# Optimization experiments

Hardware: AMD Instinct MI355X
Metric: run time of the kernel (lower is better)

## Reference

```python
import jax, jax.numpy as jnp
import numpy as np

N, E, IN_DIM, EMBED_DIM, HID_DIM = 10000, 320000, 128, 128, 64
NEG_SLOPE = 0.2


def setup_inputs() -> dict:
    key = jax.random.key(0)
    ks = jax.random.split(key, 7)
    x = jax.random.normal(ks[0], (N, IN_DIM), dtype=jnp.float32)
    edge_index = jax.random.randint(ks[1], (2, E), 0, N, dtype=jnp.int64)
    dense_w = jax.random.normal(ks[2], (IN_DIM, EMBED_DIM), dtype=jnp.float32) / np.sqrt(IN_DIM)
    dense_b = jnp.zeros((EMBED_DIM,), dtype=jnp.float32)
    gat_w = jax.random.normal(ks[3], (EMBED_DIM, HID_DIM), dtype=jnp.float32) / np.sqrt(EMBED_DIM)
    att_src = jax.random.normal(ks[4], (HID_DIM,), dtype=jnp.float32) * 0.1
    att_dst = jax.random.normal(ks[5], (HID_DIM,), dtype=jnp.float32) * 0.1
    gat_b = jnp.zeros((HID_DIM,), dtype=jnp.float32)
    return {"x": x, "edge_index": edge_index, "dense_w": dense_w, "dense_b": dense_b,
            "gat_w": gat_w, "att_src": att_src, "att_dst": att_dst, "gat_b": gat_b}


def reference(x, edge_index, dense_w, dense_b, gat_w, att_src, att_dst, gat_b):
    n = x.shape[0]
    # dense + relu
    h = jax.nn.relu(x @ dense_w + dense_b)            # [N, embed]
    # GATConv (heads=1): linear transform
    z = h @ gat_w                                     # [N, hid]
    # add self loops (PyG default)
    loops = jnp.arange(n, dtype=edge_index.dtype)
    src = jnp.concatenate([edge_index[0], loops])     # [E+N] message source j
    dst = jnp.concatenate([edge_index[1], loops])     # [E+N] message target i
    a_src = z @ att_src                               # [N]
    a_dst = z @ att_dst                               # [N]
    e = jax.nn.leaky_relu(a_src[src] + a_dst[dst], NEG_SLOPE)  # [E+N]
    # segment softmax over incoming edges of each target node
    m = jax.ops.segment_max(e, dst, num_segments=n)
    ex = jnp.exp(e - m[dst])
    denom = jax.ops.segment_sum(ex, dst, num_segments=n)
    alpha = ex / denom[dst]                           # [E+N]
    embed_x = jax.ops.segment_sum(alpha[:, None] * z[src], dst, num_segments=n) + gat_b  # [N, hid]
    # pairwise sigmoid similarity
    sim = jax.nn.sigmoid(embed_x @ embed_x.T)         # [N, N]
    return sim, embed_x
```

## Files before the change

### kernel.cpp

```cpp
#include <hip/hip_runtime.h>
#include <math.h>

#define N_NODES 10000
#define E_EDGES 320000
#define IN_DIM 128
#define EMB 128
#define HID 64
#define NEG_SLOPE 0.2f

typedef __attribute__((ext_vector_type(8))) short short8;
typedef __attribute__((ext_vector_type(4))) short short4_t;
typedef __attribute__((ext_vector_type(4))) float floatx4;

__device__ __forceinline__ short f2bf(float f) {
    unsigned u = __float_as_uint(f);
    unsigned r = u + 0x7fffu + ((u >> 16) & 1u);
    return (short)(r >> 16);
}

__global__ __launch_bounds__(256) void dense_gat_kernel(
    const float* __restrict__ x, const float* __restrict__ dw,
    const float* __restrict__ db, const float* __restrict__ gw,
    float* __restrict__ z)
{
    __shared__ float xs[16][IN_DIM];
    __shared__ float hs[16][EMB];
    const int t = threadIdx.x;
    const int row0 = blockIdx.x * 16;

    #pragma unroll
    for (int r = 0; r < 2; ++r) {
        const int idx = t + r * 256;
        const int row = idx >> 5, c4 = idx & 31;
        *(floatx4*)&xs[row][c4 * 4] =
            *(const floatx4*)&x[(row0 + row) * IN_DIM + c4 * 4];
    }
    __syncthreads();

    {
        const int col = t & 127, rb = (t >> 7) * 8;
        float acc[8];
        const float bias = db[col];
        #pragma unroll
        for (int r = 0; r < 8; ++r) acc[r] = bias;
        for (int j = 0; j < IN_DIM; ++j) {
            const float wj = dw[j * EMB + col];
            #pragma unroll
            for (int r = 0; r < 8; ++r) acc[r] = fmaf(xs[rb + r][j], wj, acc[r]);
        }
        #pragma unroll
        for (int r = 0; r < 8; ++r) hs[rb + r][col] = fmaxf(acc[r], 0.f);
    }
    __syncthreads();

    {
        const int col = t & 63, rb = (t >> 6) * 4;
        float acc[4] = {0.f, 0.f, 0.f, 0.f};
        for (int k = 0; k < EMB; ++k) {
            const float g = gw[k * HID + col];
            #pragma unroll
            for (int r = 0; r < 4; ++r) acc[r] = fmaf(hs[rb + r][k], g, acc[r]);
        }
        #pragma unroll
        for (int r = 0; r < 4; ++r) z[(row0 + rb + r) * HID + col] = acc[r];
    }
}

__global__ __launch_bounds__(256) void att_kernel(
    const float* __restrict__ z, const float* __restrict__ asv,
    const float* __restrict__ adv, float* __restrict__ a_src,
    float* __restrict__ a_dst)
{
    const int wid  = (blockIdx.x * blockDim.x + threadIdx.x) >> 6;
    const int lane = threadIdx.x & 63;
    if (wid >= N_NODES) return;
    const float zv = z[wid * HID + lane];
    float ps = zv * asv[lane];
    float pd = zv * adv[lane];
    #pragma unroll
    for (int off = 32; off > 0; off >>= 1) {
        ps += __shfl_down(ps, off, 64);
        pd += __shfl_down(pd, off, 64);
    }
    if (lane == 0) { a_src[wid] = ps; a_dst[wid] = pd; }
}

__global__ __launch_bounds__(256) void count_kernel(
    const int* __restrict__ ei, int* __restrict__ cnt)
{
    const int e = blockIdx.x * blockDim.x + threadIdx.x;
    const int total = E_EDGES + N_NODES;
    if (e >= total) return;
    int s, d;
    if (e < E_EDGES) { s = ei[e]; d = ei[E_EDGES + e]; }
    else             { s = d = e - E_EDGES; }
    if ((unsigned)s >= N_NODES || (unsigned)d >= N_NODES) return;
    atomicAdd(&cnt[d], 1);
}

__global__ __launch_bounds__(256) void scan_kernel(
    const int* __restrict__ cnt, int* __restrict__ offs, int* __restrict__ cursor)
{
    __shared__ int part[256];
    const int t = threadIdx.x;
    const int base = t * 40;
    int vals[40];
    int local = 0;
    #pragma unroll
    for (int i = 0; i < 40; ++i) {
        const int idx = base + i;
        const int c = (idx < N_NODES) ? cnt[idx] : 0;
        vals[i] = c;
        local += c;
    }
    part[t] = local;
    __syncthreads();
    for (int off = 1; off < 256; off <<= 1) {
        const int v = (t >= off) ? part[t - off] : 0;
        __syncthreads();
        part[t] += v;
        __syncthreads();
    }
    int running = (t == 0) ? 0 : part[t - 1];
    #pragma unroll
    for (int i = 0; i < 40; ++i) {
        const int idx = base + i;
        if (idx < N_NODES) { offs[idx] = running; cursor[idx] = running; }
        running += vals[i];
    }
    if (t == 255) offs[N_NODES] = running;
}

__global__ __launch_bounds__(256) void scatter_kernel(
    const int* __restrict__ ei, const float* __restrict__ a_src,
    const float* __restrict__ a_dst, int* __restrict__ cursor,
    int* __restrict__ srcs, float* __restrict__ ew)
{
    const int e = blockIdx.x * blockDim.x + threadIdx.x;
    const int total = E_EDGES + N_NODES;
    if (e >= total) return;
    int s, d;
    if (e < E_EDGES) { s = ei[e]; d = ei[E_EDGES + e]; }
    else             { s = d = e - E_EDGES; }
    if ((unsigned)s >= N_NODES || (unsigned)d >= N_NODES) return;
    float v = a_src[s] + a_dst[d];
    v = (v > 0.f) ? v : NEG_SLOPE * v;
    const float w = __expf(v);
    const int pos = atomicAdd(&cursor[d], 1);
    srcs[pos] = s;
    ew[pos]   = w;
}

__global__ __launch_bounds__(256) void aggregate_kernel(
    const int* __restrict__ offs, const int* __restrict__ srcs,
    const float* __restrict__ ew, const float* __restrict__ z,
    const float* __restrict__ gb, float* __restrict__ emb)
{
    const int wid  = (blockIdx.x * blockDim.x + threadIdx.x) >> 6;
    const int lane = threadIdx.x & 63;
    if (wid >= N_NODES) return;
    const int beg = offs[wid], end = offs[wid + 1];
    float acc = 0.f, sw = 0.f;
    for (int i = beg; i < end; ++i) {
        const int s   = srcs[i];
        const float w = ew[i];
        acc = fmaf(w, z[s * HID + lane], acc);
        sw += w;
    }
    emb[wid * HID + lane] = acc / sw + gb[lane];
}

#define SROW 72
__global__ __launch_bounds__(256) void sim_kernel(
    const float* __restrict__ emb, float* __restrict__ sim)
{
    __shared__ short As[128 * SROW];
    __shared__ short Bs[128 * SROW];
    const int t    = threadIdx.x;
    const int lane = t & 63;
    const int wave = t >> 6;
    const int wm   = (wave >> 1) * 64;
    const int wn   = (wave & 1) * 64;
    const int l15  = lane & 15;
    const int quad = lane >> 4;

    #pragma unroll
    for (int round = 0; round < 8; ++round) {
        const int idx = t + round * 256;
        const int row = idx >> 4, c4 = idx & 15;
        int gr = blockIdx.y * 128 + row; if (gr > N_NODES - 1) gr = N_NODES - 1;
        int gc = blockIdx.x * 128 + row; if (gc > N_NODES - 1) gc = N_NODES - 1;
        const floatx4 a = *(const floatx4*)&emb[gr * HID + c4 * 4];
        const floatx4 b = *(const floatx4*)&emb[gc * HID + c4 * 4];
        short4_t sa, sb;
        #pragma unroll
        for (int j = 0; j < 4; ++j) { sa[j] = f2bf(a[j]); sb[j] = f2bf(b[j]); }
        *(short4_t*)&As[row * SROW + c4 * 4] = sa;
        *(short4_t*)&Bs[row * SROW + c4 * 4] = sb;
    }
    __syncthreads();

    short8 afrag[4][2];
    #pragma unroll
    for (int ti = 0; ti < 4; ++ti)
        #pragma unroll
        for (int ks = 0; ks < 2; ++ks)
            afrag[ti][ks] = *(const short8*)&As[(wm + ti * 16 + l15) * SROW +
                                                ks * 32 + quad * 8];

    floatx4 acc[4][4];
    const floatx4 zero = {0.f, 0.f, 0.f, 0.f};
    #pragma unroll
    for (int ti = 0; ti < 4; ++ti)
        #pragma unroll
        for (int tj = 0; tj < 4; ++tj) acc[ti][tj] = zero;

    #pragma unroll
    for (int tj = 0; tj < 4; ++tj) {
        const short8 bf0 = *(const short8*)&Bs[(wn + tj * 16 + l15) * SROW + quad * 8];
        const short8 bf1 = *(const short8*)&Bs[(wn + tj * 16 + l15) * SROW + 32 + quad * 8];
        #pragma unroll
        for (int ti = 0; ti < 4; ++ti) {
            acc[ti][tj] = __builtin_amdgcn_mfma_f32_16x16x32_bf16(
                afrag[ti][0], bf0, acc[ti][tj], 0, 0, 0);
            acc[ti][tj] = __builtin_amdgcn_mfma_f32_16x16x32_bf16(
                afrag[ti][1], bf1, acc[ti][tj], 0, 0, 0);
        }
    }

    #pragma unroll
    for (int ti = 0; ti < 4; ++ti) {
        #pragma unroll
        for (int reg = 0; reg < 4; ++reg) {
            const int gr = blockIdx.y * 128 + wm + ti * 16 + quad * 4 + reg;
            if (gr >= N_NODES) continue;
            const size_t rowoff = (size_t)gr * N_NODES;
            #pragma unroll
            for (int tj = 0; tj < 4; ++tj) {
                const int gc = blockIdx.x * 128 + wn + tj * 16 + l15;
                if (gc < N_NODES) {
                    const float v = acc[ti][tj][reg];
                    sim[rowoff + gc] = __builtin_amdgcn_rcpf(1.f + __expf(-v));
                }
            }
        }
    }
}

extern "C" void kernel_launch(void* const* d_in, const int* in_sizes, int n_in,
                              void* d_out, int out_size, void* d_ws, size_t ws_size,
                              hipStream_t stream)
{
    const float* x   = (const float*)d_in[0];
    const int*   ei  = (const int*)d_in[1];
    const float* dw  = (const float*)d_in[2];
    const float* db  = (const float*)d_in[3];
    const float* gw  = (const float*)d_in[4];
    const float* asv = (const float*)d_in[5];
    const float* adv = (const float*)d_in[6];
    const float* gb  = (const float*)d_in[7];

    float* out = (float*)d_out;
    float* sim = out;
    float* emb = out + (size_t)N_NODES * N_NODES;

    const size_t need = 1350001u * sizeof(float);
    float* ws = (ws_size >= need) ? (float*)d_ws : out;
    float* z      = ws;
    float* a_src  = ws + 640000;
    float* a_dst  = ws + 650000;
    int*   cnt    = (int*)(ws + 660000);
    int*   offs   = (int*)(ws + 670000);
    int*   cursor = (int*)(ws + 680001);
    int*   srcs   = (int*)(ws + 690001);
    float* ew     = ws + 1020001;

    hipMemsetAsync(cnt, 0, N_NODES * sizeof(int), stream);

    dense_gat_kernel<<<N_NODES / 16, 256, 0, stream>>>(x, dw, db, gw, z);
    att_kernel<<<(N_NODES * 64 + 255) / 256, 256, 0, stream>>>(z, asv, adv,
                                                               a_src, a_dst);

    const int total_edges = E_EDGES + N_NODES;
    const int eb = (total_edges + 255) / 256;
    count_kernel<<<eb, 256, 0, stream>>>(ei, cnt);
    scan_kernel<<<1, 256, 0, stream>>>(cnt, offs, cursor);
    scatter_kernel<<<eb, 256, 0, stream>>>(ei, a_src, a_dst, cursor, srcs, ew);
    aggregate_kernel<<<(N_NODES * 64 + 255) / 256, 256, 0, stream>>>(
        offs, srcs, ew, z, gb, emb);

    dim3 grid((N_NODES + 127) / 128, (N_NODES + 127) / 128);
    sim_kernel<<<grid, 256, 0, stream>>>(emb, sim);
}
```

Baseline: 563.2 us.

## Exploit similarity symmetry with LDS-staged vector stores and fuse attention projection

The similarity kernel now computes only upper-triangular 128x128 tiles and writes each tile plus its transpose. Output goes through shared-memory staging so stores are coalesced float4 writes. Other changes: the attention-score dot products are fused into the dense kernel with weights tiled in LDS, the scan stages counts through LDS, the source index and edge weight are packed into one 8-byte record, and the aggregate loop is unrolled by two. Transposed stores and extra barriers add LDS traffic and sync cost.

Result: slower. 614.7 us (+9.2%).

```diff
diff --git a/kernel.cpp b/kernel.cpp
--- a/kernel.cpp
+++ b/kernel.cpp
@@ -11,6 +11,8 @@
 typedef __attribute__((ext_vector_type(8))) short short8;
 typedef __attribute__((ext_vector_type(4))) short short4_t;
 typedef __attribute__((ext_vector_type(4))) float floatx4;
+typedef __attribute__((ext_vector_type(4))) int   intx4;
+typedef __attribute__((ext_vector_type(2))) int   intx2;
 
 __device__ __forceinline__ short f2bf(float f) {
     unsigned u = __float_as_uint(f);
@@ -18,13 +20,19 @@
     return (short)(r >> 16);
 }
 
+__device__ __forceinline__ float sigmoidf_fast(float v) {
+    return __builtin_amdgcn_rcpf(1.f + __expf(-v));
+}
+
 __global__ __launch_bounds__(256) void dense_gat_kernel(
     const float* __restrict__ x, const float* __restrict__ dw,
     const float* __restrict__ db, const float* __restrict__ gw,
-    float* __restrict__ z)
+    const float* __restrict__ asv, const float* __restrict__ adv,
+    float* __restrict__ z, float* __restrict__ a_src, float* __restrict__ a_dst)
 {
     __shared__ float xs[16][IN_DIM];
     __shared__ float hs[16][EMB];
+    __shared__ float wsm[32 * 128];
     const int t = threadIdx.x;
     const int row0 = blockIdx.x * 16;
 
@@ -35,54 +43,88 @@
         *(floatx4*)&xs[row][c4 * 4] =
             *(const floatx4*)&x[(row0 + row) * IN_DIM + c4 * 4];
     }
-    __syncthreads();
-
+
+    const int col = t & 127, rb = (t >> 7) * 8;
+    float acc[8];
     {
-        const int col = t & 127, rb = (t >> 7) * 8;
-        float acc[8];
         const float bias = db[col];
         #pragma unroll
         for (int r = 0; r < 8; ++r) acc[r] = bias;
-        for (int j = 0; j < IN_DIM; ++j) {
-            const float wj = dw[j * EMB + col];
-            #pragma unroll
-            for (int r = 0; r < 8; ++r) acc[r] = fmaf(xs[rb + r][j], wj, acc[r]);
-        }
-        #pragma unroll
-        for (int r = 0; r < 8; ++r) hs[rb + r][col] = fmaxf(acc[r], 0.f);
-    }
-    __syncthreads();
-
-    {
-        const int col = t & 63, rb = (t >> 6) * 4;
-        float acc[4] = {0.f, 0.f, 0.f, 0.f};
-        for (int k = 0; k < EMB; ++k) {
-            const float g = gw[k * HID + col];
-            #pragma unroll
-            for (int r = 0; r < 4; ++r) acc[r] = fmaf(hs[rb + r][k], g, acc[r]);
-        }
-        #pragma unroll
-        for (int r = 0; r < 4; ++r) z[(row0 + rb + r) * HID + col] = acc[r];
-    }
-}
-
-__global__ __launch_bounds__(256) void att_kernel(
-    const float* __restrict__ z, const float* __restrict__ asv,
-    const float* __restrict__ adv, float* __restrict__ a_src,
-    float* __restrict__ a_dst)
-{
-    const int wid  = (blockIdx.x * blockDim.x + threadIdx.x) >> 6;
-    const int lane = threadIdx.x & 63;
-    if (wid >= N_NODES) return;
-    const float zv = z[wid * HID + lane];
-    float ps = zv * asv[lane];
-    float pd = zv * adv[lane];
-    #pragma unroll
-    for (int off = 32; off > 0; off >>= 1) {
-        ps += __shfl_down(ps, off, 64);
-        pd += __shfl_down(pd, off, 64);
-    }
-    if (lane == 0) { a_src[wid] = ps; a_dst[wid] = pd; }
+    }
+    for (int ch = 0; ch < 4; ++ch) {
+        __syncthreads();
+        #pragma unroll
+        for (int r = 0; r < 4; ++r) {
+            const int idx = t + r * 256;
+            const int row = idx >> 5, c4 = idx & 31;
+            *(floatx4*)&wsm[row * 128 + c4 * 4] =
+                *(const floatx4*)&dw[(ch * 32 + row) * EMB + c4 * 4];
+        }
+        __syncthreads();
+        #pragma unroll
+        for (int jg = 0; jg < 8; ++jg) {
+            const int jb = jg * 4;
+            floatx4 xr[8];
+            #pragma unroll
+            for (int r = 0; r < 8; ++r)
+                xr[r] = *(const floatx4*)&xs[rb + r][ch * 32 + jb];
+            float wv[4];
+            #pragma unroll
+            for (int k = 0; k < 4; ++k) wv[k] = wsm[(jb + k) * 128 + col];
+            #pragma unroll
+            for (int k = 0; k < 4; ++k)
+                #pragma unroll
+                for (int r = 0; r < 8; ++r) acc[r] = fmaf(xr[r][k], wv[k], acc[r]);
+        }
+    }
+    #pragma unroll
+    for (int r = 0; r < 8; ++r) hs[rb + r][col] = fmaxf(acc[r], 0.f);
+
+    const int col2 = t & 63, rb2 = (t >> 6) * 4;
+    float acc2[4] = {0.f, 0.f, 0.f, 0.f};
+    for (int ch = 0; ch < 2; ++ch) {
+        __syncthreads();
+        #pragma unroll
+        for (int r = 0; r < 4; ++r) {
+            const int idx = t + r * 256;
+            const int row = idx >> 4, c4 = idx & 15;
+            *(floatx4*)&wsm[row * 64 + c4 * 4] =
+                *(const floatx4*)&gw[(ch * 64 + row) * HID + c4 * 4];
+        }
+        __syncthreads();
+        #pragma unroll
+        for (int kg = 0; kg < 16; ++kg) {
+            const int kb = kg * 4;
+            floatx4 hr[4];
+            #pragma unroll
+            for (int r = 0; r < 4; ++r)
+                hr[r] = *(const floatx4*)&hs[rb2 + r][ch * 64 + kb];
+            float gv[4];
+            #pragma unroll
+            for (int k = 0; k < 4; ++k) gv[k] = wsm[(kb + k) * 64 + col2];
+            #pragma unroll
+            for (int k = 0; k < 4; ++k)
+                #pragma unroll
+                for (int r = 0; r < 4; ++r) acc2[r] = fmaf(hr[r][k], gv[k], acc2[r]);
+        }
+    }
+
+    const float as_c = asv[col2], ad_c = adv[col2];
+    #pragma unroll
+    for (int r = 0; r < 4; ++r) {
+        z[(row0 + rb2 + r) * HID + col2] = acc2[r];
+        float ps = acc2[r] * as_c;
+        float pd = acc2[r] * ad_c;
+        #pragma unroll
+        for (int off = 32; off > 0; off >>= 1) {
+            ps += __shfl_down(ps, off, 64);
+            pd += __shfl_down(pd, off, 64);
+        }
+        if ((t & 63) == 0) {
+            a_src[row0 + rb2 + r] = ps;
+            a_dst[row0 + rb2 + r] = pd;
+        }
+    }
 }
 
 __global__ __launch_bounds__(256) void count_kernel(
@@ -101,18 +143,22 @@
 __global__ __launch_bounds__(256) void scan_kernel(
     const int* __restrict__ cnt, int* __restrict__ offs, int* __restrict__ cursor)
 {
+    __shared__ int scnt[10240];
     __shared__ int part[256];
     const int t = threadIdx.x;
+    #pragma unroll
+    for (int r = 0; r < 10; ++r) {
+        const int i4 = t + r * 256;
+        intx4 v = {0, 0, 0, 0};
+        if (i4 < 2500) v = *(const intx4*)&cnt[i4 * 4];
+        *(intx4*)&scnt[i4 * 4] = v;
+    }
+    __syncthreads();
     const int base = t * 40;
     int vals[40];
     int local = 0;
     #pragma unroll
-    for (int i = 0; i < 40; ++i) {
-        const int idx = base + i;
-        const int c = (idx < N_NODES) ? cnt[idx] : 0;
-        vals[i] = c;
-        local += c;
-    }
+    for (int i = 0; i < 40; ++i) { vals[i] = scnt[base + i]; local += vals[i]; }
     part[t] = local;
     __syncthreads();
     for (int off = 1; off < 256; off <<= 1) {
@@ -134,7 +180,7 @@
 __global__ __launch_bounds__(256) void scatter_kernel(
     const int* __restrict__ ei, const float* __restrict__ a_src,
     const float* __restrict__ a_dst, int* __restrict__ cursor,
-    int* __restrict__ srcs, float* __restrict__ ew)
+    intx2* __restrict__ se)
 {
     const int e = blockIdx.x * blockDim.x + threadIdx.x;
     const int total = E_EDGES + N_NODES;
@@ -147,24 +193,38 @@
     v = (v > 0.f) ? v : NEG_SLOPE * v;
     const float w = __expf(v);
     const int pos = atomicAdd(&cursor[d], 1);
-    srcs[pos] = s;
-    ew[pos]   = w;
+    intx2 p;
+    p[0] = s;
+    p[1] = __float_as_int(w);
+    se[pos] = p;
 }
 
 __global__ __launch_bounds__(256) void aggregate_kernel(
-    const int* __restrict__ offs, const int* __restrict__ srcs,
-    const float* __restrict__ ew, const float* __restrict__ z,
-    const float* __restrict__ gb, float* __restrict__ emb)
+    const int* __restrict__ offs, const intx2* __restrict__ se,
+    const float* __restrict__ z, const float* __restrict__ gb,
+    float* __restrict__ emb)
 {
     const int wid  = (blockIdx.x * blockDim.x + threadIdx.x) >> 6;
     const int lane = threadIdx.x & 63;
     if (wid >= N_NODES) return;
     const int beg = offs[wid], end = offs[wid + 1];
     float acc = 0.f, sw = 0.f;
-    for (int i = beg; i < end; ++i) {
-        const int s   = srcs[i];
-        const float w = ew[i];
-        acc = fmaf(w, z[s * HID + lane], acc);
+    int i = beg;
+    for (; i + 2 <= end; i += 2) {
+        const intx2 p0 = se[i];
+        const intx2 p1 = se[i + 1];
+        const float z0 = z[p0[0] * HID + lane];
+        const float z1 = z[p1[0] * HID + lane];
+        const float w0 = __int_as_float(p0[1]);
+        const float w1 = __int_as_float(p1[1]);
+        acc = fmaf(w0, z0, acc);
+        acc = fmaf(w1, z1, acc);
+        sw += w0 + w1;
+    }
+    if (i < end) {
+        const intx2 p = se[i];
+        const float w = __int_as_float(p[1]);
+        acc = fmaf(w, z[p[0] * HID + lane], acc);
         sw += w;
     }
     emb[wid * HID + lane] = acc / sw + gb[lane];
@@ -184,12 +244,19 @@
     const int l15  = lane & 15;
     const int quad = lane >> 4;
 
+    int bi, bj;
+    {
+        const int gx = blockIdx.x, gy = blockIdx.y;
+        if (gy <= gx) { bi = gy; bj = gx; }
+        else          { bi = 40 + gx; bj = 79 + gx - gy; }
+    }
+
     #pragma unroll
     for (int round = 0; round < 8; ++round) {
         const int idx = t + round * 256;
         const int row = idx >> 4, c4 = idx & 15;
-        int gr = blockIdx.y * 128 + row; if (gr > N_NODES - 1) gr = N_NODES - 1;
-        int gc = blockIdx.x * 128 + row; if (gc > N_NODES - 1) gc = N_NODES - 1;
+        int gr = bi * 128 + row; if (gr > N_NODES - 1) gr = N_NODES - 1;
+        int gc = bj * 128 + row; if (gc > N_NODES - 1) gc = N_NODES - 1;
         const floatx4 a = *(const floatx4*)&emb[gr * HID + c4 * 4];
         const floatx4 b = *(const floatx4*)&emb[gc * HID + c4 * 4];
         short4_t sa, sb;
@@ -227,21 +294,49 @@
                 afrag[ti][1], bf1, acc[ti][tj], 0, 0, 0);
         }
     }
+    __syncthreads();
+
+    float* const scr0 = (float*)As;
+    float* const scr1 = (float*)Bs;
+    const int srow0 = (wave >> 1) * 16 + quad * 4;
 
     #pragma unroll
     for (int ti = 0; ti < 4; ++ti) {
-        #pragma unroll
-        for (int reg = 0; reg < 4; ++reg) {
-            const int gr = blockIdx.y * 128 + wm + ti * 16 + quad * 4 + reg;
-            if (gr >= N_NODES) continue;
-            const size_t rowoff = (size_t)gr * N_NODES;
-            #pragma unroll
-            for (int tj = 0; tj < 4; ++tj) {
-                const int gc = blockIdx.x * 128 + wn + tj * 16 + l15;
-                if (gc < N_NODES) {
-                    const float v = acc[ti][tj][reg];
-                    sim[rowoff + gc] = __builtin_amdgcn_rcpf(1.f + __expf(-v));
-                }
+        float* const scr = (ti & 1) ? scr1 : scr0;
+        #pragma unroll
+        for (int reg = 0; reg < 4; ++reg)
+            #pragma unroll
+            for (int tj = 0; tj < 4; ++tj)
+                scr[(srow0 + reg) * 132 + wn + tj * 16 + l15] =
+                    sigmoidf_fast(acc[ti][tj][reg]);
+        __syncthreads();
+
+        #pragma unroll
+        for (int round = 0; round < 4; ++round) {
+            const int idx = t + round * 256;
+            const int rr = idx >> 5, c4 = idx & 31;
+            const floatx4 v4 = *(const floatx4*)&scr[rr * 132 + c4 * 4];
+            const int grow = bi * 128 +
+                ((rr < 16) ? (ti * 16 + rr) : (64 + ti * 16 + rr - 16));
+            const int gcol = bj * 128 + c4 * 4;
+            if (grow < N_NODES && gcol < N_NODES)
+                *(floatx4*)&sim[(unsigned)grow * N_NODES + gcol] = v4;
+        }
+        if (bi != bj) {
+            #pragma unroll
+            for (int round = 0; round < 4; ++round) {
+                const int idx = t + round * 256;
+                const int kq  = idx & 3;
+                const int gcl = (idx >> 2) & 127;
+                const int blk = idx >> 9;
+                floatx4 v4;
+                #pragma unroll
+                for (int m = 0; m < 4; ++m)
+                    v4[m] = scr[(blk * 16 + kq * 4 + m) * 132 + gcl];
+                const int trow = bj * 128 + gcl;
+                const int tcol = bi * 128 + blk * 64 + ti * 16 + kq * 4;
+                if (trow < N_NODES && tcol < N_NODES)
+                    *(floatx4*)&sim[(unsigned)trow * N_NODES + tcol] = v4;
             }
         }
     }
@@ -264,7 +359,7 @@
     float* sim = out;
     float* emb = out + (size_t)N_NODES * N_NODES;
 
-    const size_t need = 1350001u * sizeof(float);
+    const size_t need = 1350002u * sizeof(float);
     float* ws = (ws_size >= need) ? (float*)d_ws : out;
     float* z      = ws;
     float* a_src  = ws + 640000;
@@ -272,23 +367,21 @@
     int*   cnt    = (int*)(ws + 660000);
     int*   offs   = (int*)(ws + 670000);
     int*   cursor = (int*)(ws + 680001);
-    int*   srcs   = (int*)(ws + 690001);
-    float* ew     = ws + 1020001;
+    intx2* se     = (intx2*)(ws + 690002);
 
     hipMemsetAsync(cnt, 0, N_NODES * sizeof(int), stream);
 
-    dense_gat_kernel<<<N_NODES / 16, 256, 0, stream>>>(x, dw, db, gw, z);
-    att_kernel<<<(N_NODES * 64 + 255) / 256, 256, 0, stream>>>(z, asv, adv,
-                                                               a_src, a_dst);
+    dense_gat_kernel<<<N_NODES / 16, 256, 0, stream>>>(x, dw, db, gw, asv, adv,
+                                                       z, a_src, a_dst);
 
     const int total_edges = E_EDGES + N_NODES;
     const int eb = (total_edges + 255) / 256;
     count_kernel<<<eb, 256, 0, stream>>>(ei, cnt);
     scan_kernel<<<1, 256, 0, stream>>>(cnt, offs, cursor);
-    scatter_kernel<<<eb, 256, 0, stream>>>(ei, a_src, a_dst, cursor, srcs, ew);
+    scatter_kernel<<<eb, 256, 0, stream>>>(ei, a_src, a_dst, cursor, se);
     aggregate_kernel<<<(N_NODES * 64 + 255) / 256, 256, 0, stream>>>(
-        offs, srcs, ew, z, gb, emb);
-
-    dim3 grid((N_NODES + 127) / 128, (N_NODES + 127) / 128);
+        offs, se, z, gb, emb);
+
+    dim3 grid(79, 40);
     sim_kernel<<<grid, 256, 0, stream>>>(emb, sim);
 }
```
